# Kernel tuning notes

Measured on AMD Instinct MI355X. Metric: run time of the kernel, lower is better.

Reference implementation:

```python
import jax, jax.numpy as jnp
import numpy as np

B, S, D = 2, 2048, 512
P, T, MAP_H = 13, 5, 64


def setup_inputs() -> dict:
    key = jax.random.key(0)
    ks = jax.random.split(key, 8)
    s = 0.02
    return {
        "hidden_states": jax.random.normal(ks[0], (B, S, D), jnp.float32),
        "ln_gamma": jnp.ones((D,), jnp.float32),
        "ln_beta": jnp.zeros((D,), jnp.float32),
        "W_in": jax.random.normal(ks[1], (D, P * D), jnp.float32) * s,
        "b_in": jnp.zeros((P * D,), jnp.float32),
        "W_map1": jax.random.normal(ks[2], (D, MAP_H), jnp.float32) * s,
        "b_map1": jnp.zeros((MAP_H,), jnp.float32),
        "W_map2": jax.random.normal(ks[3], (MAP_H, T), jnp.float32) * s,
        "b_map2": jnp.zeros((T,), jnp.float32),
        "log_tau": jnp.linspace(0.0, 4.0, T).astype(jnp.float32),
        "mix": jax.random.normal(ks[4], (P, T), jnp.float32) / float(P * T),
        "W_out": jax.random.normal(ks[5], (D, D), jnp.float32) * s,
        "b_out": jnp.zeros((D,), jnp.float32),
        "scale": jnp.float32(1e-3),
        "h_prev": jnp.zeros((B, P, T, D), jnp.float32),
        "position_offset": 0,
    }


def _forward(hidden_states, ln_gamma, ln_beta, W_in, b_in, W_map1, b_map1,
             W_map2, b_map2, log_tau, mix, W_out, b_out, scale, h_prev):
    b, s_len, d = hidden_states.shape
    p, t = mix.shape
    # pre-norm (LayerNorm, eps=1e-5)
    mu = jnp.mean(hidden_states, -1, keepdims=True)
    var = jnp.var(hidden_states, -1, keepdims=True)
    xn = (hidden_states - mu) * jax.lax.rsqrt(var + 1e-5) * ln_gamma + ln_beta
    # per-protofilament input drive: [B,S,P,D]
    u = (xn @ W_in + b_in).reshape(b, s_len, p, d)
    # liquid (input-dependent) decay per time scale: [B,S,T]
    gate = jax.nn.sigmoid(jnp.tanh(xn @ W_map1 + b_map1) @ W_map2 + b_map2)
    alpha = jnp.exp(-gate / jnp.exp(log_tau))  # [B,S,T]

    def step(h, inp):
        u_t, a_t = inp                      # [B,P,D], [B,T]
        a = a_t[:, None, :, None]           # broadcast over P and D
        h = a * h + (1.0 - a) * u_t[:, :, None, :]   # [B,P,T,D]
        y = jnp.einsum('bptd,pt->bd', h, mix)        # mix protofilaments/time scales
        return h, y

    _, ys = jax.lax.scan(step, h_prev,
                         (jnp.moveaxis(u, 1, 0), jnp.moveaxis(alpha, 1, 0)))
    mt_out = jnp.moveaxis(ys, 0, 1) @ W_out + b_out  # [B,S,D]
    return hidden_states + scale * mt_out


def reference(hidden_states, ln_gamma, ln_beta, W_in, b_in, W_map1, b_map1,
              W_map2, b_map2, log_tau, mix, W_out, b_out, scale, h_prev,
              position_offset):
    return _forward(hidden_states, ln_gamma, ln_beta, W_in, b_in, W_map1,
                    b_map1, W_map2, b_map2, log_tau, mix, W_out, b_out,
                    scale, h_prev)
```

## Files before the change

kernel.cpp:

```cpp
#include <hip/hip_runtime.h>
#include <hip/hip_bf16.h>
#include <stdint.h>

#define BB 2
#define SS 2048
#define DD 512
#define PP 13
#define TT 5
#define MH 64
#define MM (BB*SS)
#define NV (TT*DD)
#define KK 512
#define CHUNK 16
#define NCH (SS/CHUNK)

typedef __attribute__((ext_vector_type(4))) float f32x4;
typedef __attribute__((ext_vector_type(8))) short s8v;
typedef unsigned int u32;
typedef __attribute__((address_space(3))) u32 lds_u32_t;
typedef __attribute__((address_space(1))) const u32 glb_u32_t;

__device__ __forceinline__ float bf2f(unsigned short u){
  union { unsigned int i; float f; } c; c.i = ((unsigned int)u) << 16; return c.f;
}
__device__ __forceinline__ unsigned short f2bf(float f){
  union { float f; unsigned int i; } c; c.f = f;
  unsigned int x = c.i;
  unsigned int r = (x + 0x7fffu + ((x >> 16) & 1u)) >> 16;
  return (unsigned short)r;
}
__device__ __forceinline__ void gld16(unsigned short* l, const unsigned short* g){
  __builtin_amdgcn_global_load_lds((glb_u32_t*)g, (lds_u32_t*)l, 16, 0, 0);
}

__global__ __launch_bounds__(256) void k_prep_ln(
    const float* __restrict__ hs,
    const float* __restrict__ gamma, const float* __restrict__ beta,
    const float* __restrict__ W_in, const float* __restrict__ b_in,
    const float* __restrict__ mix,  const float* __restrict__ W_out,
    const float* __restrict__ W1,
    unsigned short* __restrict__ xn_bf,
    unsigned short* __restrict__ W_vT, float* __restrict__ b_v,
    unsigned short* __restrict__ W_outT, unsigned short* __restrict__ W1T)
{
  int blk = blockIdx.x;
  if (blk < 1024){
    int tid = threadIdx.x;
    int lane = tid & 63;
    int row = blk*4 + (tid>>6);
    const float* x = hs + (size_t)row*DD + lane*8;
    float4 v0 = *(const float4*)x;
    float4 v1 = *(const float4*)(x+4);
    float s  = v0.x+v0.y+v0.z+v0.w + v1.x+v1.y+v1.z+v1.w;
    float sq = v0.x*v0.x+v0.y*v0.y+v0.z*v0.z+v0.w*v0.w
             + v1.x*v1.x+v1.y*v1.y+v1.z*v1.z+v1.w*v1.w;
    #pragma unroll
    for (int o=32;o>0;o>>=1){ s += __shfl_xor(s,o); sq += __shfl_xor(sq,o); }
    float mu   = s  * (1.f/DD);
    float var  = sq * (1.f/DD) - mu*mu;
    float rstd = rsqrtf(var + 1e-5f);
    float4 g0 = *(const float4*)(gamma + lane*8);
    float4 g1 = *(const float4*)(gamma + lane*8 + 4);
    float4 b0 = *(const float4*)(beta  + lane*8);
    float4 b1 = *(const float4*)(beta  + lane*8 + 4);
    union { unsigned short us[8]; uint4 u; } pk;
    pk.us[0] = f2bf((v0.x-mu)*rstd*g0.x + b0.x);
    pk.us[1] = f2bf((v0.y-mu)*rstd*g0.y + b0.y);
    pk.us[2] = f2bf((v0.z-mu)*rstd*g0.z + b0.z);
    pk.us[3] = f2bf((v0.w-mu)*rstd*g0.w + b0.w);
    pk.us[4] = f2bf((v1.x-mu)*rstd*g1.x + b1.x);
    pk.us[5] = f2bf((v1.y-mu)*rstd*g1.y + b1.y);
    pk.us[6] = f2bf((v1.z-mu)*rstd*g1.z + b1.z);
    pk.us[7] = f2bf((v1.w-mu)*rstd*g1.w + b1.w);
    *(uint4*)(xn_bf + (size_t)row*DD + lane*8) = pk.u;
  } else if (blk < 1152){
    int idx = (blk-1024) * 256 + threadIdx.x;
    int d  = idx & (DD-1);
    int k0 = idx >> 9;
    float mx[PP][TT];
    #pragma unroll
    for (int p=0;p<PP;++p)
      #pragma unroll
      for (int t=0;t<TT;++t) mx[p][t] = mix[p*TT+t];
    float acc[TT][8];
    #pragma unroll
    for (int t=0;t<TT;++t)
      #pragma unroll
      for (int j=0;j<8;++j) acc[t][j] = 0.f;
    #pragma unroll
    for (int j=0;j<8;++j){
      int k = k0*8 + j;
      const float* wrow = W_in + (size_t)k * (PP*DD) + d;
      #pragma unroll
      for (int p=0;p<PP;++p){
        float w = wrow[p*DD];
        #pragma unroll
        for (int t=0;t<TT;++t) acc[t][j] += mx[p][t]*w;
      }
    }
    #pragma unroll
    for (int t=0;t<TT;++t){
      union { unsigned short us[8]; uint4 u; } pk;
      #pragma unroll
      for (int j=0;j<8;++j) pk.us[j] = f2bf(acc[t][j]);
      *(uint4*)(W_vT + ((size_t)(t*DD+d))*KK + k0*8) = pk.u;
    }
    if (k0 == 0){
      #pragma unroll
      for (int t=0;t<TT;++t){
        float s = 0.f;
        #pragma unroll
        for (int p=0;p<PP;++p) s += mx[p][t]*b_in[p*DD+d];
        b_v[t*DD+d] = s;
      }
    }
  } else if (blk < 1280){
    int idx = (blk-1152)*256 + threadIdx.x;
    int n  = idx & (DD-1);
    int k0 = idx >> 9;
    union { unsigned short us[8]; uint4 u; } pk;
    #pragma unroll
    for (int j=0;j<8;++j) pk.us[j] = f2bf(W_out[(size_t)(k0*8+j)*DD + n]);
    *(uint4*)(W_outT + (size_t)n*KK + k0*8) = pk.u;
  } else {
    int idx = (blk-1280)*256 + threadIdx.x;
    int n  = idx >> 6;
    int k0 = idx & 63;
    union { unsigned short us[8]; uint4 u; } pk;
    #pragma unroll
    for (int j=0;j<8;++j) pk.us[j] = f2bf(W1[(size_t)(k0*8+j)*MH + n]);
    *(uint4*)(W1T + (size_t)n*KK + k0*8) = pk.u;
  }
}

__global__ __launch_bounds__(256) void k_gate(
    const unsigned short* __restrict__ xn,
    const unsigned short* __restrict__ W1T,
    const float* __restrict__ b1, const float* __restrict__ W2,
    const float* __restrict__ b2, const float* __restrict__ ltau,
    float* __restrict__ alpha)
{
  __shared__ unsigned short lA[2][64*32];
  __shared__ unsigned short lB[2][64*32];
  int bm = blockIdx.x;
  int tid = threadIdx.x, lane = tid & 63, w = tid >> 6;
  int lr = lane & 15, kq = lane >> 4;
  const uint8_t* gA = (const uint8_t*)(xn  + (size_t)(bm*64 + w*16 + (lane>>2))*KK) + (lane&3)*16;
  const uint8_t* gB = (const uint8_t*)(W1T + (size_t)(        w*16 + (lane>>2))*KK) + (lane&3)*16;
  f32x4 acc[4];
  #pragma unroll
  for (int ni=0;ni<4;++ni) acc[ni] = (f32x4){0.f,0.f,0.f,0.f};

  auto stage = [&](int buf, int kt){
    int off = kt*64;
    gld16(&lA[buf][(w*16)*32], (const unsigned short*)(gA + off));
    gld16(&lB[buf][(w*16)*32], (const unsigned short*)(gB + off));
  };
  auto compute = [&](int buf){
    union { uint4 u; s8v v; } af, bfr[4];
    af.u = *(const uint4*)&lA[buf][(w*16+lr)*32 + kq*8];
    #pragma unroll
    for (int ni=0;ni<4;++ni) bfr[ni].u = *(const uint4*)&lB[buf][(ni*16+lr)*32 + kq*8];
    #pragma unroll
    for (int ni=0;ni<4;++ni)
      acc[ni] = __builtin_amdgcn_mfma_f32_16x16x32_bf16(af.v, bfr[ni].v, acc[ni], 0,0,0);
  };

  stage(0, 0);
  __syncthreads();
  #pragma unroll
  for (int kt=1; kt<16; ++kt){
    stage(kt&1, kt);
    compute((kt&1)^1);
    __syncthreads();
  }
  compute(1);

  float z1[4][4];
  #pragma unroll
  for (int ni=0;ni<4;++ni){
    float bb = b1[ni*16+lr];
    #pragma unroll
    for (int r=0;r<4;++r) z1[r][ni] = tanhf(acc[ni][r] + bb);
  }
  float et[TT];
  #pragma unroll
  for (int t=0;t<TT;++t) et[t] = expf(-ltau[t]);
  float a[4][TT];
  #pragma unroll
  for (int t=0;t<TT;++t){
    float w2[4];
    #pragma unroll
    for (int ni=0;ni<4;++ni) w2[ni] = W2[(ni*16+lr)*TT + t];
    #pragma unroll
    for (int r=0;r<4;++r){
      float p = z1[r][0]*w2[0] + z1[r][1]*w2[1] + z1[r][2]*w2[2] + z1[r][3]*w2[3];
      #pragma unroll
      for (int o=8;o>0;o>>=1) p += __shfl_xor(p, o);
      float z2 = p + b2[t];
      float gate = 1.f/(1.f + expf(-z2));
      a[r][t] = expf(-gate * et[t]);
    }
  }
  if (lr < TT){
    int t = lr;
    #pragma unroll
    for (int r=0;r<4;++r){
      int row = bm*64 + w*16 + kq*4 + r;
      alpha[(size_t)row*TT + t] = a[r][t];
    }
  }
}

template<int BN, int NDIM, bool OUTEPI>
__global__ __launch_bounds__(256) void k_gemm(
    const unsigned short* __restrict__ A,
    const unsigned short* __restrict__ Bt,
    const float* __restrict__ bias,
    const float* __restrict__ hidden,
    const float* __restrict__ scale_p,
    float* __restrict__ outF,
    unsigned short* __restrict__ outBf)
{
  constexpr int NI  = (BN == 128) ? 4 : 2;
  constexpr int WNT = BN / 2;
  __shared__ unsigned short lA[2][128*32];
  __shared__ unsigned short lB[2][BN*32];
  int bn = blockIdx.x, bm = blockIdx.y;
  int tid  = threadIdx.x;
  int lane = tid & 63;
  int w    = tid >> 6;
  int wm = w >> 1, wn = w & 1;
  f32x4 acc[4][NI];
  #pragma unroll
  for (int i=0;i<4;++i)
    #pragma unroll
    for (int j=0;j<NI;++j) acc[i][j] = (f32x4){0.f,0.f,0.f,0.f};

  const uint8_t* gA = (const uint8_t*)(A + (size_t)(bm*128 + w*32 + (lane>>2))*KK) + (lane&3)*16;
  const uint8_t* gB;
  if constexpr (BN == 128) gB = (const uint8_t*)(Bt + (size_t)(bn*BN + w*32 + (lane>>2))*KK) + (lane&3)*16;
  else                     gB = (const uint8_t*)(Bt + (size_t)(bn*BN + w*16 + (lane>>2))*KK) + (lane&3)*16;
  int lr = lane & 15, kq = lane >> 4;

  auto stage = [&](int buf, int kt){
    int off = kt*64;
    gld16(&lA[buf][(w*32)*32],    (const unsigned short*)(gA + off));
    gld16(&lA[buf][(w*32+16)*32], (const unsigned short*)(gA + (size_t)16*KK*2 + off));
    if constexpr (BN == 128){
      gld16(&lB[buf][(w*32)*32],    (const unsigned short*)(gB + off));
      gld16(&lB[buf][(w*32+16)*32], (const unsigned short*)(gB + (size_t)16*KK*2 + off));
    } else {
      gld16(&lB[buf][(w*16)*32],    (const unsigned short*)(gB + off));
    }
  };
  auto compute = [&](int buf){
    union { uint4 u; s8v v; } af[4], bfr[NI];
    #pragma unroll
    for (int mi=0;mi<4;++mi) af[mi].u  = *(const uint4*)&lA[buf][(wm*64+mi*16+lr)*32 + kq*8];
    #pragma unroll
    for (int ni=0;ni<NI;++ni) bfr[ni].u = *(const uint4*)&lB[buf][(wn*WNT+ni*16+lr)*32 + kq*8];
    #pragma unroll
    for (int mi=0;mi<4;++mi)
      #pragma unroll
      for (int ni=0;ni<NI;++ni)
        acc[mi][ni] = __builtin_amdgcn_mfma_f32_16x16x32_bf16(af[mi].v, bfr[ni].v, acc[mi][ni], 0,0,0);
  };

  stage(0, 0);
  __syncthreads();
  #pragma unroll
  for (int kt=1; kt<16; ++kt){
    stage(kt&1, kt);
    compute((kt&1)^1);
    __syncthreads();
  }
  compute(1);

  float sc = 0.f;
  if constexpr (OUTEPI) sc = *scale_p;
  #pragma unroll
  for (int mi=0;mi<4;++mi){
    #pragma unroll
    for (int ni=0;ni<NI;++ni){
      int row = bm*128 + wm*64 + mi*16 + kq*4;
      int col = bn*BN  + wn*WNT + ni*16 + lr;
      float bs = bias[col];
      f32x4 c = acc[mi][ni];
      #pragma unroll
      for (int r=0;r<4;++r){
        float val = c[r] + bs;
        size_t off = (size_t)(row+r)*NDIM + col;
        if constexpr (OUTEPI) outF[off] = hidden[off] + sc*val;
        else                  outBf[off] = f2bf(val);
      }
    }
  }
}

__global__ __launch_bounds__(320) void k_scan_a(
    const float* __restrict__ alpha,
    unsigned short* __restrict__ vg,
    float* __restrict__ L, float* __restrict__ PA)
{
  int blk = blockIdx.x;
  int c = blk & (NCH-1), b = blk >> 7;
  int tid = threadIdx.x;
  int t  = tid >> 6;
  int d8 = tid & 63;
  __shared__ float sAl[CHUNK*TT];
  if (tid < CHUNK*TT) sAl[tid] = alpha[(size_t)(b*SS + c*CHUNK)*TT + tid];
  __syncthreads();
  unsigned short* vp = vg + (size_t)(b*SS + c*CHUNK)*NV + t*DD + d8*8;
  uint4 vv[CHUNK];
  #pragma unroll
  for (int s2=0;s2<CHUNK;++s2) vv[s2] = *(const uint4*)(vp + (size_t)s2*NV);
  float g[8];
  #pragma unroll
  for (int j=0;j<8;++j) g[j] = 0.f;
  float pa = 1.f;
  #pragma unroll
  for (int s2=0;s2<CHUNK;++s2){
    float a = sAl[s2*TT+t], om = 1.f - a;
    const unsigned short* pv = (const unsigned short*)&vv[s2];
    union { unsigned short us[8]; uint4 u; } o;
    #pragma unroll
    for (int j=0;j<8;++j){ g[j] = a*g[j] + om*bf2f(pv[j]); o.us[j] = f2bf(g[j]); }
    *(uint4*)(vp + (size_t)s2*NV) = o.u;
    pa *= a;
  }
  float* Lp = L + ((size_t)(b*TT+t)*NCH + c)*DD + d8*8;
  *(float4*)Lp     = (float4){g[0],g[1],g[2],g[3]};
  *(float4*)(Lp+4) = (float4){g[4],g[5],g[6],g[7]};
  if (d8 == 0) PA[(size_t)(b*TT+t)*NCH + c] = pa;
}

__global__ __launch_bounds__(512) void k_scan_b(
    const float* __restrict__ mix,
    const float* __restrict__ h_prev,
    const float* __restrict__ PA,
    const float* __restrict__ L,
    float* __restrict__ Gc)
{
  int blk = blockIdx.x;
  int t = blk % TT, b = blk / TT;
  int d = threadIdx.x;
  __shared__ float sP[NCH];
  if (d < NCH) sP[d] = PA[(size_t)(b*TT+t)*NCH + d];
  __syncthreads();
  float carry = 0.f;
  #pragma unroll
  for (int p=0;p<PP;++p)
    carry += mix[p*TT+t] * h_prev[((size_t)(b*PP+p)*TT + t)*DD + d];
  const float* Lp = L  + (size_t)(b*TT+t)*NCH*DD + d;
  float*       gc = Gc + (size_t)(b*TT+t)*NCH*DD + d;
  float buf[8], nbuf[8];
  #pragma unroll
  for (int j=0;j<8;++j) buf[j] = Lp[(size_t)j*DD];
  for (int c0=0;c0<NCH;c0+=8){
    if (c0+8 < NCH){
      #pragma unroll
      for (int j=0;j<8;++j) nbuf[j] = Lp[(size_t)(c0+8+j)*DD];
    }
    #pragma unroll
    for (int j=0;j<8;++j){
      gc[(size_t)(c0+j)*DD] = carry;
      carry = sP[c0+j]*carry + buf[j];
    }
    #pragma unroll
    for (int j=0;j<8;++j) buf[j] = nbuf[j];
  }
}

__global__ __launch_bounds__(256) void k_scan_c(
    const float* __restrict__ alpha,
    const unsigned short* __restrict__ g_loc,
    const float* __restrict__ Gc,
    unsigned short* __restrict__ ybf)
{
  int blk = blockIdx.x;
  int c = blk & (NCH-1), b = blk >> 7;
  int tid = threadIdx.x;
  int s4 = tid >> 6;
  int d8 = tid & 63;
  __shared__ float sAl[CHUNK*TT];
  if (tid < CHUNK*TT) sAl[tid] = alpha[(size_t)(b*SS + c*CHUNK)*TT + tid];
  __syncthreads();
  float ca[TT][8];
  #pragma unroll
  for (int t=0;t<TT;++t){
    const float* gp = Gc + ((size_t)(b*TT+t)*NCH + c)*DD + d8*8;
    float4 c0 = *(const float4*)gp;
    float4 c1 = *(const float4*)(gp+4);
    ca[t][0]=c0.x; ca[t][1]=c0.y; ca[t][2]=c0.z; ca[t][3]=c0.w;
    ca[t][4]=c1.x; ca[t][5]=c1.y; ca[t][6]=c1.z; ca[t][7]=c1.w;
  }
  float pr[TT];
  #pragma unroll
  for (int t=0;t<TT;++t){
    float p = 1.f;
    for (int j=0;j<s4*4;++j) p *= sAl[j*TT+t];
    pr[t] = p;
  }
  const unsigned short* gl = g_loc + (size_t)(b*SS + c*CHUNK)*NV + d8*8;
  unsigned short* yp = ybf + (size_t)(b*SS + c*CHUNK)*DD + d8*8;
  #pragma unroll
  for (int i=0;i<4;++i){
    int s2 = s4*4 + i;
    float y[8];
    #pragma unroll
    for (int j=0;j<8;++j) y[j] = 0.f;
    #pragma unroll
    for (int t=0;t<TT;++t){
      pr[t] *= sAl[s2*TT+t];
      uint4 gv = *(const uint4*)(gl + (size_t)s2*NV + t*DD);
      const unsigned short* gp = (const unsigned short*)&gv;
      #pragma unroll
      for (int j=0;j<8;++j) y[j] += bf2f(gp[j]) + pr[t]*ca[t][j];
    }
    union { unsigned short us[8]; uint4 u; } o;
    #pragma unroll
    for (int j=0;j<8;++j) o.us[j] = f2bf(y[j]);
    *(uint4*)(yp + (size_t)s2*DD) = o.u;
  }
}

extern "C" void kernel_launch(void* const* d_in, const int* in_sizes, int n_in,
                              void* d_out, int out_size, void* d_ws, size_t ws_size,
                              hipStream_t stream)
{
  (void)in_sizes; (void)n_in; (void)out_size; (void)ws_size;
  const float* hs     = (const float*)d_in[0];
  const float* gamma  = (const float*)d_in[1];
  const float* beta   = (const float*)d_in[2];
  const float* W_in   = (const float*)d_in[3];
  const float* b_in   = (const float*)d_in[4];
  const float* W1     = (const float*)d_in[5];
  const float* b1     = (const float*)d_in[6];
  const float* W2     = (const float*)d_in[7];
  const float* b2     = (const float*)d_in[8];
  const float* ltau   = (const float*)d_in[9];
  const float* mix    = (const float*)d_in[10];
  const float* W_out  = (const float*)d_in[11];
  const float* b_out  = (const float*)d_in[12];
  const float* scale  = (const float*)d_in[13];
  const float* h_prev = (const float*)d_in[14];
  float* out = (float*)d_out;

  uint8_t* w = (uint8_t*)d_ws;
  unsigned short* xn   = (unsigned short*)(w);
  unsigned short* WvT  = (unsigned short*)(w + 4194304);
  unsigned short* WoT  = (unsigned short*)(w + 6815744);
  float* alphaB        = (float*)(w + 7340032);
  float* b_v           = (float*)(w + 7421952);
  float* PA            = (float*)(w + 7432192);
  float* L             = (float*)(w + 7437312);
  float* Gc            = (float*)(w + 10058752);
  unsigned short* vg   = (unsigned short*)(w + 12680192);
  unsigned short* ybf  = (unsigned short*)(w + 33651712);
  unsigned short* W1T  = ybf;

  hipLaunchKernelGGL(k_prep_ln, dim3(1296), dim3(256), 0, stream,
                     hs, gamma, beta, W_in, b_in, mix, W_out, W1,
                     xn, WvT, b_v, WoT, W1T);
  hipLaunchKernelGGL(k_gate, dim3(MM/64), dim3(256), 0, stream, xn, W1T, b1, W2, b2, ltau, alphaB);
  hipLaunchKernelGGL((k_gemm<128,NV,false>), dim3(NV/128, MM/128), dim3(256), 0, stream,
                     xn, WvT, b_v, nullptr, nullptr, nullptr, vg);
  hipLaunchKernelGGL(k_scan_a, dim3(BB*NCH), dim3(320), 0, stream, alphaB, vg, L, PA);
  hipLaunchKernelGGL(k_scan_b, dim3(BB*TT), dim3(512), 0, stream, mix, h_prev, PA, L, Gc);
  hipLaunchKernelGGL(k_scan_c, dim3(BB*NCH), dim3(256), 0, stream, alphaB, vg, Gc, ybf);
  hipLaunchKernelGGL((k_gemm<64,DD,true>), dim3(DD/64, MM/128), dim3(256), 0, stream,
                     ybf, WoT, b_out, hs, scale, out, nullptr);
}
```

Before: 82.95 us.

## Swizzle GEMM LDS and tiles, pipeline waits, reduce scan-local outputs in-kernel

The GEMM gets an XOR-swizzled LDS layout to avoid bank conflicts, a block-index swizzle for L2 locality, and explicit vmcnt waits so the next stage's loads stay in flight while the current tile is computed. The first scan pass now sums the per-timescale local states over T inside LDS and writes a single [B,S,D] bf16 tensor instead of writing back the full T*D intermediate. The last scan pass then reads that compact tensor, which cuts global traffic. The cost is extra LDS use and barriers in scan_a, plus hand-tuned wait counts that depend on how many loads each stage issues.

```diff
diff --git a/kernel.cpp b/kernel.cpp
--- a/kernel.cpp
+++ b/kernel.cpp
@@ -62,16 +62,16 @@
     float4 g0 = *(const float4*)(gamma + lane*8);
     float4 g1 = *(const float4*)(gamma + lane*8 + 4);
     float4 b0 = *(const float4*)(beta  + lane*8);
-    float4 b1 = *(const float4*)(beta  + lane*8 + 4);
+    float4 b1v = *(const float4*)(beta + lane*8 + 4);
     union { unsigned short us[8]; uint4 u; } pk;
     pk.us[0] = f2bf((v0.x-mu)*rstd*g0.x + b0.x);
     pk.us[1] = f2bf((v0.y-mu)*rstd*g0.y + b0.y);
     pk.us[2] = f2bf((v0.z-mu)*rstd*g0.z + b0.z);
     pk.us[3] = f2bf((v0.w-mu)*rstd*g0.w + b0.w);
-    pk.us[4] = f2bf((v1.x-mu)*rstd*g1.x + b1.x);
-    pk.us[5] = f2bf((v1.y-mu)*rstd*g1.y + b1.y);
-    pk.us[6] = f2bf((v1.z-mu)*rstd*g1.z + b1.z);
-    pk.us[7] = f2bf((v1.w-mu)*rstd*g1.w + b1.w);
+    pk.us[4] = f2bf((v1.x-mu)*rstd*g1.x + b1v.x);
+    pk.us[5] = f2bf((v1.y-mu)*rstd*g1.y + b1v.y);
+    pk.us[6] = f2bf((v1.z-mu)*rstd*g1.z + b1v.z);
+    pk.us[7] = f2bf((v1.w-mu)*rstd*g1.w + b1v.w);
     *(uint4*)(xn_bf + (size_t)row*DD + lane*8) = pk.u;
   } else if (blk < 1152){
     int idx = (blk-1024) * 256 + threadIdx.x;
@@ -213,7 +213,7 @@
 }
 
 template<int BN, int NDIM, bool OUTEPI>
-__global__ __launch_bounds__(256) void k_gemm(
+__global__ __launch_bounds__(256, 4) void k_gemm(
     const unsigned short* __restrict__ A,
     const unsigned short* __restrict__ Bt,
     const float* __restrict__ bias,
@@ -224,9 +224,13 @@
 {
   constexpr int NI  = (BN == 128) ? 4 : 2;
   constexpr int WNT = BN / 2;
+  constexpr int NLD = (BN == 128) ? 4 : 3;
   __shared__ unsigned short lA[2][128*32];
   __shared__ unsigned short lB[2][BN*32];
-  int bn = blockIdx.x, bm = blockIdx.y;
+  int bid = blockIdx.y * gridDim.x + blockIdx.x;
+  int nwg = gridDim.x * gridDim.y;
+  int swz = (bid & 7) * (nwg >> 3) + (bid >> 3);
+  int bn = swz % gridDim.x, bm = swz / gridDim.x;
   int tid  = threadIdx.x;
   int lane = tid & 63;
   int w    = tid >> 6;
@@ -237,11 +241,14 @@
     #pragma unroll
     for (int j=0;j<NI;++j) acc[i][j] = (f32x4){0.f,0.f,0.f,0.f};
 
-  const uint8_t* gA = (const uint8_t*)(A + (size_t)(bm*128 + w*32 + (lane>>2))*KK) + (lane&3)*16;
+  int srow  = lane >> 2;
+  int slotS = (lane & 3) ^ (srow & 3);
+  const uint8_t* gA = (const uint8_t*)(A + (size_t)(bm*128 + w*32 + srow)*KK) + slotS*16;
   const uint8_t* gB;
-  if constexpr (BN == 128) gB = (const uint8_t*)(Bt + (size_t)(bn*BN + w*32 + (lane>>2))*KK) + (lane&3)*16;
-  else                     gB = (const uint8_t*)(Bt + (size_t)(bn*BN + w*16 + (lane>>2))*KK) + (lane&3)*16;
+  if constexpr (BN == 128) gB = (const uint8_t*)(Bt + (size_t)(bn*BN + w*32 + srow)*KK) + slotS*16;
+  else                     gB = (const uint8_t*)(Bt + (size_t)(bn*BN + w*16 + srow)*KK) + slotS*16;
   int lr = lane & 15, kq = lane >> 4;
+  int kqs = kq ^ (lr & 3);
 
   auto stage = [&](int buf, int kt){
     int off = kt*64;
@@ -257,9 +264,9 @@
   auto compute = [&](int buf){
     union { uint4 u; s8v v; } af[4], bfr[NI];
     #pragma unroll
-    for (int mi=0;mi<4;++mi) af[mi].u  = *(const uint4*)&lA[buf][(wm*64+mi*16+lr)*32 + kq*8];
-    #pragma unroll
-    for (int ni=0;ni<NI;++ni) bfr[ni].u = *(const uint4*)&lB[buf][(wn*WNT+ni*16+lr)*32 + kq*8];
+    for (int mi=0;mi<4;++mi) af[mi].u  = *(const uint4*)&lA[buf][(wm*64+mi*16+lr)*32 + kqs*8];
+    #pragma unroll
+    for (int ni=0;ni<NI;++ni) bfr[ni].u = *(const uint4*)&lB[buf][(wn*WNT+ni*16+lr)*32 + kqs*8];
     #pragma unroll
     for (int mi=0;mi<4;++mi)
       #pragma unroll
@@ -268,14 +275,22 @@
   };
 
   stage(0, 0);
-  __syncthreads();
-  #pragma unroll
-  for (int kt=1; kt<16; ++kt){
-    stage(kt&1, kt);
-    compute((kt&1)^1);
-    __syncthreads();
-  }
-  compute(1);
+  #pragma unroll
+  for (int kt=0; kt<16; ++kt){
+    if (kt < 15){
+      stage((kt+1)&1, kt+1);
+      if constexpr (NLD == 4) asm volatile("s_waitcnt vmcnt(4)" ::: "memory");
+      else                    asm volatile("s_waitcnt vmcnt(3)" ::: "memory");
+    } else {
+      asm volatile("s_waitcnt vmcnt(0)" ::: "memory");
+    }
+    __builtin_amdgcn_sched_barrier(0);
+    __builtin_amdgcn_s_barrier();
+    __builtin_amdgcn_sched_barrier(0);
+    compute(kt&1);
+    __builtin_amdgcn_sched_barrier(0);
+    __builtin_amdgcn_s_barrier();
+  }
 
   float sc = 0.f;
   if constexpr (OUTEPI) sc = *scale_p;
@@ -300,8 +315,9 @@
 
 __global__ __launch_bounds__(320) void k_scan_a(
     const float* __restrict__ alpha,
-    unsigned short* __restrict__ vg,
-    float* __restrict__ L, float* __restrict__ PA)
+    const unsigned short* __restrict__ v,
+    float* __restrict__ L, float* __restrict__ PA,
+    unsigned short* __restrict__ yloc)
 {
   int blk = blockIdx.x;
   int c = blk & (NCH-1), b = blk >> 7;
@@ -309,25 +325,51 @@
   int t  = tid >> 6;
   int d8 = tid & 63;
   __shared__ float sAl[CHUNK*TT];
+  __shared__ unsigned short yl[TT][8][DD];
   if (tid < CHUNK*TT) sAl[tid] = alpha[(size_t)(b*SS + c*CHUNK)*TT + tid];
   __syncthreads();
-  unsigned short* vp = vg + (size_t)(b*SS + c*CHUNK)*NV + t*DD + d8*8;
-  uint4 vv[CHUNK];
-  #pragma unroll
-  for (int s2=0;s2<CHUNK;++s2) vv[s2] = *(const uint4*)(vp + (size_t)s2*NV);
+  const unsigned short* vp = v + (size_t)(b*SS + c*CHUNK)*NV + t*DD + d8*8;
   float g[8];
   #pragma unroll
   for (int j=0;j<8;++j) g[j] = 0.f;
   float pa = 1.f;
   #pragma unroll
-  for (int s2=0;s2<CHUNK;++s2){
-    float a = sAl[s2*TT+t], om = 1.f - a;
-    const unsigned short* pv = (const unsigned short*)&vv[s2];
-    union { unsigned short us[8]; uint4 u; } o;
-    #pragma unroll
-    for (int j=0;j<8;++j){ g[j] = a*g[j] + om*bf2f(pv[j]); o.us[j] = f2bf(g[j]); }
-    *(uint4*)(vp + (size_t)s2*NV) = o.u;
-    pa *= a;
+  for (int half=0; half<2; ++half){
+    uint4 vv[8];
+    #pragma unroll
+    for (int s=0;s<8;++s) vv[s] = *(const uint4*)(vp + (size_t)(half*8+s)*NV);
+    #pragma unroll
+    for (int s=0;s<8;++s){
+      float a = sAl[(half*8+s)*TT+t], om = 1.f - a;
+      const unsigned short* pv = (const unsigned short*)&vv[s];
+      union { unsigned short us[8]; uint4 u; } o;
+      #pragma unroll
+      for (int j=0;j<8;++j){ g[j] = a*g[j] + om*bf2f(pv[j]); o.us[j] = f2bf(g[j]); }
+      *(uint4*)&yl[t][s][d8*8] = o.u;
+      pa *= a;
+    }
+    __syncthreads();
+    if (t < 4){
+      #pragma unroll
+      for (int ii=0; ii<2; ++ii){
+        int s = t*2 + ii;
+        float y[8];
+        #pragma unroll
+        for (int j=0;j<8;++j) y[j] = 0.f;
+        #pragma unroll
+        for (int tt=0;tt<TT;++tt){
+          uint4 gv = *(const uint4*)&yl[tt][s][d8*8];
+          const unsigned short* gp = (const unsigned short*)&gv;
+          #pragma unroll
+          for (int j=0;j<8;++j) y[j] += bf2f(gp[j]);
+        }
+        union { unsigned short us[8]; uint4 u; } o;
+        #pragma unroll
+        for (int j=0;j<8;++j) o.us[j] = f2bf(y[j]);
+        *(uint4*)(yloc + (size_t)(b*SS + c*CHUNK + half*8 + s)*DD + d8*8) = o.u;
+      }
+    }
+    __syncthreads();
   }
   float* Lp = L + ((size_t)(b*TT+t)*NCH + c)*DD + d8*8;
   *(float4*)Lp     = (float4){g[0],g[1],g[2],g[3]};
@@ -374,7 +416,7 @@
 
 __global__ __launch_bounds__(256) void k_scan_c(
     const float* __restrict__ alpha,
-    const unsigned short* __restrict__ g_loc,
+    const unsigned short* __restrict__ yloc,
     const float* __restrict__ Gc,
     unsigned short* __restrict__ ybf)
 {
@@ -402,26 +444,26 @@
     for (int j=0;j<s4*4;++j) p *= sAl[j*TT+t];
     pr[t] = p;
   }
-  const unsigned short* gl = g_loc + (size_t)(b*SS + c*CHUNK)*NV + d8*8;
-  unsigned short* yp = ybf + (size_t)(b*SS + c*CHUNK)*DD + d8*8;
+  const unsigned short* yp = yloc + (size_t)(b*SS + c*CHUNK)*DD + d8*8;
+  unsigned short* op = ybf + (size_t)(b*SS + c*CHUNK)*DD + d8*8;
   #pragma unroll
   for (int i=0;i<4;++i){
     int s2 = s4*4 + i;
+    uint4 yv = *(const uint4*)(yp + (size_t)s2*DD);
+    const unsigned short* yq = (const unsigned short*)&yv;
     float y[8];
     #pragma unroll
-    for (int j=0;j<8;++j) y[j] = 0.f;
+    for (int j=0;j<8;++j) y[j] = bf2f(yq[j]);
     #pragma unroll
     for (int t=0;t<TT;++t){
       pr[t] *= sAl[s2*TT+t];
-      uint4 gv = *(const uint4*)(gl + (size_t)s2*NV + t*DD);
-      const unsigned short* gp = (const unsigned short*)&gv;
-      #pragma unroll
-      for (int j=0;j<8;++j) y[j] += bf2f(gp[j]) + pr[t]*ca[t][j];
+      #pragma unroll
+      for (int j=0;j<8;++j) y[j] += pr[t]*ca[t][j];
     }
     union { unsigned short us[8]; uint4 u; } o;
     #pragma unroll
     for (int j=0;j<8;++j) o.us[j] = f2bf(y[j]);
-    *(uint4*)(yp + (size_t)s2*DD) = o.u;
+    *(uint4*)(op + (size_t)s2*DD) = o.u;
   }
 }
 
@@ -459,6 +501,7 @@
   unsigned short* vg   = (unsigned short*)(w + 12680192);
   unsigned short* ybf  = (unsigned short*)(w + 33651712);
   unsigned short* W1T  = ybf;
+  unsigned short* yloc = xn;
 
   hipLaunchKernelGGL(k_prep_ln, dim3(1296), dim3(256), 0, stream,
                      hs, gamma, beta, W_in, b_in, mix, W_out, W1,
@@ -466,9 +509,9 @@
   hipLaunchKernelGGL(k_gate, dim3(MM/64), dim3(256), 0, stream, xn, W1T, b1, W2, b2, ltau, alphaB);
   hipLaunchKernelGGL((k_gemm<128,NV,false>), dim3(NV/128, MM/128), dim3(256), 0, stream,
                      xn, WvT, b_v, nullptr, nullptr, nullptr, vg);
-  hipLaunchKernelGGL(k_scan_a, dim3(BB*NCH), dim3(320), 0, stream, alphaB, vg, L, PA);
+  hipLaunchKernelGGL(k_scan_a, dim3(BB*NCH), dim3(320), 0, stream, alphaB, vg, L, PA, yloc);
   hipLaunchKernelGGL(k_scan_b, dim3(BB*TT), dim3(512), 0, stream, mix, h_prev, PA, L, Gc);
-  hipLaunchKernelGGL(k_scan_c, dim3(BB*NCH), dim3(256), 0, stream, alphaB, vg, Gc, ybf);
+  hipLaunchKernelGGL(k_scan_c, dim3(BB*NCH), dim3(256), 0, stream, alphaB, yloc, Gc, ybf);
   hipLaunchKernelGGL((k_gemm<64,DD,true>), dim3(DD/64, MM/128), dim3(256), 0, stream,
                      ybf, WoT, b_out, hs, scale, out, nullptr);
 }
```

After: 76.86 us. -7.3%, faster.
